# Optimization experiments

Measured on AMD Instinct MI355X. Metric: run time of the kernel, lower is better.

## Reference

```python
import math
import jax, jax.numpy as jnp
import numpy as np

N = 20000      # nodes
E = 320000     # edges
D_IN = 256
D_OUT = 256
H = 8
DK = D_OUT // H  # 32


def setup_inputs() -> dict:
    key = jax.random.key(0)
    ks = jax.random.split(key, 16)
    h = jax.random.normal(ks[0], (N, D_IN), dtype=jnp.float32)
    src = jax.random.randint(ks[1], (E,), 0, N, dtype=jnp.int32)
    dst = jax.random.randint(ks[2], (E,), 0, N, dtype=jnp.int32)
    s = 1.0 / math.sqrt(D_IN)
    Wk = jax.random.uniform(ks[3], (D_OUT, D_IN), jnp.float32, -s, s)
    bk = jnp.zeros((D_OUT,), jnp.float32)
    Wq = jax.random.uniform(ks[4], (D_OUT, D_IN), jnp.float32, -s, s)
    bq = jnp.zeros((D_OUT,), jnp.float32)
    Wv = jax.random.uniform(ks[5], (D_OUT, D_IN), jnp.float32, -s, s)
    bv = jnp.zeros((D_OUT,), jnp.float32)
    so = 1.0 / math.sqrt(D_OUT)
    Wa = jax.random.uniform(ks[6], (D_OUT, D_OUT), jnp.float32, -so, so)
    ba = jnp.zeros((D_OUT,), jnp.float32)
    # xavier_uniform over [n_rel=1, H, DK, DK]; fan_in = fan_out = DK
    bound = math.sqrt(6.0 / (DK + DK))
    rel_att = jax.random.uniform(ks[7], (H, DK, DK), jnp.float32, -bound, bound)
    rel_msg = jax.random.uniform(ks[8], (H, DK, DK), jnp.float32, -bound, bound)
    rel_pri = jnp.ones((H,), jnp.float32)
    skip = jnp.ones((), jnp.float32)
    return {"h": h, "src": src, "dst": dst, "Wk": Wk, "bk": bk, "Wq": Wq,
            "bq": bq, "Wv": Wv, "bv": bv, "Wa": Wa, "ba": ba,
            "rel_att": rel_att, "rel_msg": rel_msg, "rel_pri": rel_pri,
            "skip": skip}


def reference(h, src, dst, Wk, bk, Wq, bq, Wv, bv, Wa, ba, rel_att, rel_msg, rel_pri, skip):
    n = h.shape[0]
    sqrt_dk = math.sqrt(DK)
    # per-node projections, [N, H, DK]
    k = (h @ Wk.T + bk).reshape(n, H, DK)
    q = (h @ Wq.T + bq).reshape(n, H, DK)
    v = (h @ Wv.T + bv).reshape(n, H, DK)
    # relation-specific transforms (single relation, index 0)
    k = jnp.einsum('nhd,hde->nhe', k, rel_att)
    v = jnp.einsum('nhd,hde->nhe', v, rel_msg)
    # edge-wise dot-product score: v_dot_u(q_dst, k_src) -> [E, H]
    score = jnp.einsum('ehd,ehd->eh', q[dst], k[src]) * rel_pri / sqrt_dk
    # edge softmax normalized by dst
    m = jax.ops.segment_max(score, dst, num_segments=n)          # [N, H]
    ex = jnp.exp(score - m[dst])
    z = jax.ops.segment_sum(ex, dst, num_segments=n)             # [N, H]
    attn = ex / z[dst]                                           # [E, H]
    # weighted message aggregation: sum_e attn * v_src -> [N, H, DK]
    agg = jax.ops.segment_sum(v[src] * attn[:, :, None], dst, num_segments=n)
    t = agg.reshape(n, D_OUT)
    trans = t @ Wa.T + ba                                        # dropout = eval identity
    alpha = jax.nn.sigmoid(skip)
    return trans * alpha + h * (1.0 - alpha)
```

## Files before the change

kernel.cpp:

```cpp
#include <hip/hip_runtime.h>
#include <hip/hip_bf16.h>
#include <math.h>


#define NN   20000
#define NE   320000
#define MPAD 20096
#define DSTRIDE 96

typedef unsigned short u16;
typedef unsigned char  u8;
typedef __bf16 bf16x8 __attribute__((ext_vector_type(8)));
typedef u16    u16x8  __attribute__((ext_vector_type(8)));
typedef float  f32x4  __attribute__((ext_vector_type(4)));

__device__ __forceinline__ float bf2f(u16 x) {
    union { float f; unsigned u; } c; c.u = ((unsigned)x) << 16; return c.f;
}
__device__ __forceinline__ u16 f2bf(float f) {
    union { float f; unsigned u; } c; c.f = f;
    unsigned r = c.u + 0x7fffu + ((c.u >> 16) & 1u);
    return (u16)(r >> 16);
}

#if __has_builtin(__builtin_amdgcn_cvt_pk_fp8_f32) && __has_builtin(__builtin_amdgcn_cvt_pk_f32_fp8)
#define HWFP8 1
#else
#define HWFP8 0
#endif

__device__ __forceinline__ u8 f2fp8(float x) {
#if HWFP8
    return (u8)(__builtin_amdgcn_cvt_pk_fp8_f32(x, x, 0, false) & 0xff);
#else
    if (x != x) return 0x7f;
    unsigned sg = (x < 0.f) ? 0x80u : 0u;
    float a = fabsf(x); if (a > 448.f) a = 448.f;
    if (a < 0.015625f) {
        int m = (int)rintf(a * 512.f);
        if (m > 7) return (u8)(sg | 0x08);
        return (u8)(sg | m);
    }
    int e; (void)frexpf(a, &e);
    int p = e - 1;
    float mant = a * exp2f((float)(-p));
    int m = (int)rintf((mant - 1.f) * 8.f);
    int ef = p + 7;
    if (m == 8) { m = 0; ef++; }
    if (ef > 15) { ef = 15; m = 6; }
    return (u8)(sg | (ef << 3) | m);
#endif
}

__device__ __forceinline__ void fp8x4_dec(unsigned w, float* o) {
#if HWFP8
    auto lo = __builtin_amdgcn_cvt_pk_f32_fp8(w, false);
    auto hi = __builtin_amdgcn_cvt_pk_f32_fp8(w, true);
    o[0] = lo[0]; o[1] = lo[1]; o[2] = hi[0]; o[3] = hi[1];
#else
    #pragma unroll
    for (int j = 0; j < 4; ++j) {
        u8 b = (w >> (8 * j)) & 0xff;
        unsigned e = (b >> 3) & 15, m = b & 7;
        float v;
        if (e) { union { unsigned u; float f; } c; c.u = ((e + 120) << 23) | (m << 20); v = c.f; }
        else v = (float)m * 0.001953125f;
        o[j] = (b & 0x80) ? -v : v;
    }
#endif
}

__device__ __forceinline__ float fast_exp2(float x) {
#if __has_builtin(__builtin_amdgcn_exp2f)
    return __builtin_amdgcn_exp2f(x);
#else
    return exp2f(x);
#endif
}

__global__ void prep0(const float* __restrict__ Wq, const float* __restrict__ bq,
                      const float* __restrict__ Wk, const float* __restrict__ bk,
                      const float* __restrict__ Wv, const float* __restrict__ bv,
                      const float* __restrict__ Wa,
                      const float* __restrict__ rel_att, const float* __restrict__ rel_msg,
                      const float* __restrict__ rel_pri,
                      u16* __restrict__ W_all, float* __restrict__ b_eff,
                      u16* __restrict__ Wa_bf, int* __restrict__ cnt)
{
    const int bid = blockIdx.x, t = threadIdx.x;
    if (bid < 20) {
        const int i = bid * 256 + t;
        if (i < 5024) *(int4*)(cnt + i * 4) = make_int4(0, 0, 0, 0);
    } else if (bid < 788) {
        const int row = bid - 20, col = t;
        float val;
        if (row < 256) {
            val = Wq[row * 256 + col];
            if (col == 0) b_eff[row] = bq[row];
        } else {
            const int i = row - 256, g = i >> 7, o = i & 127;
            const bool isk = (o < 64);
            const int d = 64 * g + (isk ? o : o - 64);
            const int hh = d >> 5, e = d & 31;
            if (isk) {
                const float s = rel_pri[hh] * 0.17677669529663687f * 1.4426950408889634f;
                float acc = 0.f;
                for (int dd = 0; dd < 32; ++dd)
                    acc += rel_att[hh * 1024 + dd * 32 + e] * Wk[(hh * 32 + dd) * 256 + col];
                val = acc * s;
                if (col == 0) {
                    float b = 0.f;
                    for (int dd = 0; dd < 32; ++dd) b += rel_att[hh * 1024 + dd * 32 + e] * bk[hh * 32 + dd];
                    b_eff[row] = b * s;
                }
            } else {
                float acc = 0.f;
                for (int dd = 0; dd < 32; ++dd)
                    acc += rel_msg[hh * 1024 + dd * 32 + e] * Wv[(hh * 32 + dd) * 256 + col];
                val = acc;
                if (col == 0) {
                    float b = 0.f;
                    for (int dd = 0; dd < 32; ++dd) b += rel_msg[hh * 1024 + dd * 32 + e] * bv[hh * 32 + dd];
                    b_eff[row] = b;
                }
            }
        }
        W_all[row * 256 + col] = f2bf(val);
    } else {
        const int idx = (bid - 788) * 256 + t;
        Wa_bf[idx] = f2bf(Wa[idx]);
    }
}

__global__ __launch_bounds__(256) void gemm_qkv(
    const float* __restrict__ h, const u16* __restrict__ B,
    const float* __restrict__ bias, const int* __restrict__ src, const int* __restrict__ dst,
    u16* __restrict__ qb, u8* __restrict__ kv8, int* __restrict__ cnt, int* __restrict__ esrc)
{
    if (blockIdx.x >= 960) {
        const int e = (blockIdx.x - 960) * 256 + threadIdx.x;
        if (e < NE) {
            const int d = dst[e];
            const int p = atomicAdd(&cnt[d], 1);
            if (p < DSTRIDE) esrc[d * DSTRIDE + p] = src[e];
        }
        return;
    }
    const int xcd = blockIdx.x & 7, slot = blockIdx.x >> 3;
    const int rb = (slot % 20) * 8 + xcd;
    const int cb = slot / 20;
    if (rb >= 157) return;
    __shared__ u16 LDS[128 * 128];
    u16* At = LDS;
    u16* Bt = LDS + 128 * 64;
    const int t = threadIdx.x;
    const int wave = t >> 6, lane = t & 63;
    const int row0 = rb * 128, col0 = cb * 128;
    const int wm = (wave >> 1) * 64, wn = (wave & 1) * 64;
    const int cl = lane & 15, rh = lane >> 4;
    const int srow = t >> 3;
    const int lchunk = t & 7;
    const int swz = srow & 7;

    f32x4 acc[4][4] = {};
    float4 a0[4], a1[4];
    u16x8 bz[4];

    auto LOAD = [&](int k0) {
        #pragma unroll
        for (int r = 0; r < 4; ++r) {
            const int grow = row0 + r * 32 + srow;
            if (grow < NN) {
                a0[r] = *(const float4*)(h + (size_t)grow * 256 + k0 + lchunk * 8);
                a1[r] = *(const float4*)(h + (size_t)grow * 256 + k0 + lchunk * 8 + 4);
            } else {
                a0[r] = make_float4(0.f, 0.f, 0.f, 0.f);
                a1[r] = make_float4(0.f, 0.f, 0.f, 0.f);
            }
            bz[r] = *(const u16x8*)(B + (size_t)(col0 + r * 32 + srow) * 256 + k0 + lchunk * 8);
        }
    };
    auto COMMIT = [&]() {
        #pragma unroll
        for (int r = 0; r < 4; ++r) {
            u16x8 w8;
            w8[0] = f2bf(a0[r].x); w8[1] = f2bf(a0[r].y); w8[2] = f2bf(a0[r].z); w8[3] = f2bf(a0[r].w);
            w8[4] = f2bf(a1[r].x); w8[5] = f2bf(a1[r].y); w8[6] = f2bf(a1[r].z); w8[7] = f2bf(a1[r].w);
            *(u16x8*)&At[(r * 32 + srow) * 64 + (lchunk ^ swz) * 8] = w8;
            *(u16x8*)&Bt[(r * 32 + srow) * 64 + (lchunk ^ swz) * 8] = bz[r];
        }
    };

    LOAD(0);
    COMMIT();
    __syncthreads();
    #pragma unroll
    for (int ki = 0; ki < 4; ++ki) {
        if (ki < 3) LOAD((ki + 1) * 64);
        #pragma unroll
        for (int kk = 0; kk < 2; ++kk) {
            const int kc = kk * 4;
            bf16x8 af[4], bb[4];
            #pragma unroll
            for (int m = 0; m < 4; ++m) {
                const int ar = wm + 16 * m + cl;
                af[m] = *(const bf16x8*)&At[ar * 64 + (((kc + rh) ^ (ar & 7)) * 8)];
            }
            #pragma unroll
            for (int n = 0; n < 4; ++n) {
                const int br = wn + 16 * n + cl;
                bb[n] = *(const bf16x8*)&Bt[br * 64 + (((kc + rh) ^ (br & 7)) * 8)];
            }
            #pragma unroll
            for (int m = 0; m < 4; ++m)
                #pragma unroll
                for (int n = 0; n < 4; ++n)
                    acc[m][n] = __builtin_amdgcn_mfma_f32_16x16x32_bf16(af[m], bb[n], acc[m][n], 0, 0, 0);
        }
        __syncthreads();
        if (ki < 3) {
            COMMIT();
            __syncthreads();
        }
    }

    if (cb < 2) {
        #pragma unroll
        for (int n = 0; n < 4; ++n) {
            const int col = wn + 16 * n + cl;
            const float bv = bias[col0 + col];
            #pragma unroll
            for (int m = 0; m < 4; ++m) {
                const int rowb = wm + 16 * m + 4 * rh;
                #pragma unroll
                for (int r = 0; r < 4; ++r) {
                    const int row = rowb + r;
                    LDS[row * 128 + ((((col >> 3) ^ (row & 15)) << 3) | (col & 7))] =
                        f2bf(acc[m][n][r] + bv);
                }
            }
        }
        __syncthreads();
        #pragma unroll
        for (int it = 0; it < 8; ++it) {
            const int u = it * 256 + t;
            const int row = u >> 4, lc = u & 15;
            *(u16x8*)(qb + (size_t)(row0 + row) * 256 + col0 + lc * 8) =
                *(const u16x8*)&LDS[row * 128 + ((lc ^ (row & 15)) << 3)];
        }
    } else {
        u8* Cs8 = (u8*)LDS;
        const int g = cb - 2;
        #pragma unroll
        for (int n = 0; n < 4; ++n) {
            const int col = wn + 16 * n + cl;
            const float bv = bias[col0 + col];
            const int o = col & 63;
            const int p = ((o >> 3) << 4) + ((col < 64) ? 0 : 8) + (o & 7);
            #pragma unroll
            for (int m = 0; m < 4; ++m) {
                const int rowb = wm + 16 * m + 4 * rh;
                #pragma unroll
                for (int r = 0; r < 4; ++r) {
                    const int row = rowb + r;
                    Cs8[row * 128 + ((((p >> 3) ^ (row & 15)) << 3) | (p & 7))] =
                        f2fp8(acc[m][n][r] + bv);
                }
            }
        }
        __syncthreads();
        #pragma unroll
        for (int it = 0; it < 4; ++it) {
            const int u = it * 256 + t;
            const int row = u >> 3, un = u & 7;
            const uint2 a = *(const uint2*)&Cs8[row * 128 + (((2 * un) ^ (row & 15)) << 3)];
            const uint2 b = *(const uint2*)&Cs8[row * 128 + (((2 * un + 1) ^ (row & 15)) << 3)];
            *(uint4*)(kv8 + (size_t)(row0 + row) * 512 + g * 128 + un * 16) =
                make_uint4(a.x, a.y, b.x, b.y);
        }
    }
}

__global__ __launch_bounds__(256) void gemm_out(
    const u16* __restrict__ A, const u16* __restrict__ B,
    const float* __restrict__ bias, const float* __restrict__ hres,
    const float* __restrict__ skip, float* __restrict__ C)
{
    const int xcd = blockIdx.x & 7, slot = blockIdx.x >> 3;
    const int rb = (slot % 40) * 8 + xcd;
    const int cbo = slot / 40;
    if (rb >= 314) return;
    __shared__ u16 At[64 * 64];
    __shared__ u16 Bt[64 * 64];
    const int t = threadIdx.x;
    const int wave = t >> 6, lane = t & 63;
    const int row0 = rb * 64, col0 = cbo * 64;
    const int wm = (wave >> 1) * 32, wn = (wave & 1) * 32;
    const int cl = lane & 15, rh = lane >> 4;
    const int srow = t >> 3;
    const int lchunk = t & 7;
    const int swz = srow & 7;

    f32x4 acc[2][2] = {};
    u16x8 az[2], bz[2];

    auto LOAD = [&](int k0) {
        #pragma unroll
        for (int r = 0; r < 2; ++r) {
            az[r] = *(const u16x8*)(A + (size_t)(row0 + r * 32 + srow) * 256 + k0 + lchunk * 8);
            bz[r] = *(const u16x8*)(B + (size_t)(col0 + r * 32 + srow) * 256 + k0 + lchunk * 8);
        }
    };
    auto COMMIT = [&]() {
        #pragma unroll
        for (int r = 0; r < 2; ++r) {
            *(u16x8*)&At[(r * 32 + srow) * 64 + (lchunk ^ swz) * 8] = az[r];
            *(u16x8*)&Bt[(r * 32 + srow) * 64 + (lchunk ^ swz) * 8] = bz[r];
        }
    };

    LOAD(0);
    COMMIT();
    __syncthreads();
    #pragma unroll
    for (int ki = 0; ki < 4; ++ki) {
        if (ki < 3) LOAD((ki + 1) * 64);
        #pragma unroll
        for (int kk = 0; kk < 2; ++kk) {
            const int kc = kk * 4;
            bf16x8 af[2], bb[2];
            #pragma unroll
            for (int m = 0; m < 2; ++m) {
                const int ar = wm + 16 * m + cl;
                af[m] = *(const bf16x8*)&At[ar * 64 + (((kc + rh) ^ (ar & 7)) * 8)];
            }
            #pragma unroll
            for (int n = 0; n < 2; ++n) {
                const int br = wn + 16 * n + cl;
                bb[n] = *(const bf16x8*)&Bt[br * 64 + (((kc + rh) ^ (br & 7)) * 8)];
            }
            #pragma unroll
            for (int m = 0; m < 2; ++m)
                #pragma unroll
                for (int n = 0; n < 2; ++n)
                    acc[m][n] = __builtin_amdgcn_mfma_f32_16x16x32_bf16(af[m], bb[n], acc[m][n], 0, 0, 0);
        }
        __syncthreads();
        if (ki < 3) {
            COMMIT();
            __syncthreads();
        }
    }
    const float alpha = 1.f / (1.f + __expf(-skip[0]));
    const float beta = 1.f - alpha;
    #pragma unroll
    for (int n = 0; n < 2; ++n) {
        const int col = col0 + wn + 16 * n + cl;
        const float bv = bias[col];
        #pragma unroll
        for (int m = 0; m < 2; ++m) {
            const int rowb = row0 + wm + 16 * m + 4 * rh;
            #pragma unroll
            for (int r = 0; r < 4; ++r) {
                const int row = rowb + r;
                if (row < NN)
                    C[(size_t)row * 256 + col] =
                        (acc[m][n][r] + bv) * alpha + hres[(size_t)row * 256 + col] * beta;
            }
        }
    }
}

__device__ __forceinline__ void agg_w(uint4 w, const float* qf, float& z, float* acc)
{
    float kf[8], vf[8];
    fp8x4_dec(w.x, kf); fp8x4_dec(w.y, kf + 4);
    float s = 0.f;
    #pragma unroll
    for (int j = 0; j < 8; ++j) s += qf[j] * kf[j];
    s += __shfl_xor(s, 1);
    s += __shfl_xor(s, 2);
    const float ex = fast_exp2(s);
    z += ex;
    fp8x4_dec(w.z, vf); fp8x4_dec(w.w, vf + 4);
    #pragma unroll
    for (int j = 0; j < 8; ++j) acc[j] += ex * vf[j];
}

__global__ __launch_bounds__(256) void aggregate(
    const u16* __restrict__ qb, const u8* __restrict__ kv8, const int* __restrict__ cnt,
    const int* __restrict__ esrc, u16* __restrict__ tout)
{
    const int wid = blockIdx.x * 4 + (threadIdx.x >> 6);
    const int lane = threadIdx.x & 63;
    const int half = lane >> 5, sl = lane & 31;
    if (wid >= MPAD) return;
    if (wid >= NN) {
        if (half == 0) *(u16x8*)(tout + (size_t)wid * 256 + sl * 8) = (u16x8)0;
        return;
    }
    const u16x8 qv = *(const u16x8*)(qb + (size_t)wid * 256 + sl * 8);
    float qf[8];
    #pragma unroll
    for (int j = 0; j < 8; ++j) qf[j] = bf2f(qv[j]);
    float acc[8] = {0.f, 0.f, 0.f, 0.f, 0.f, 0.f, 0.f, 0.f};
    float z = 0.f;
    const int dcnt = min(cnt[wid], DSTRIDE);
    const int e0 = wid * DSTRIDE;
    for (int c0 = 0; c0 < dcnt; c0 += 64) {
        const int cn = min(64, dcnt - c0);
        const int jj = c0 + lane;
        const int myid = (jj < dcnt) ? esrc[e0 + jj] : 0;
        const int nfull = cn & ~15;
        int i = 0;
        for (; i < nfull; i += 16) {
            int idv[8];
            uint4 wreg[8];
            #pragma unroll
            for (int j = 0; j < 8; ++j) idv[j] = __shfl(myid, i + 2 * j + half);
            #pragma unroll
            for (int j = 0; j < 8; ++j)
                wreg[j] = *(const uint4*)(kv8 + (size_t)idv[j] * 512 + sl * 16);
            #pragma unroll
            for (int j = 0; j < 8; ++j) agg_w(wreg[j], qf, z, acc);
        }
        for (; i < cn; i += 2) {
            const int ii = i + half;
            const int id = __shfl(myid, ii);
            if (ii < cn) {
                const uint4 w = *(const uint4*)(kv8 + (size_t)id * 512 + sl * 16);
                agg_w(w, qf, z, acc);
            }
        }
    }
    #pragma unroll
    for (int j = 0; j < 8; ++j) acc[j] += __shfl_xor(acc[j], 32);
    z += __shfl_xor(z, 32);
    if (half == 0) {
        const float rz = (z > 0.f) ? 1.f / z : 0.f;
        u16x8 o;
        #pragma unroll
        for (int j = 0; j < 8; ++j) o[j] = f2bf(acc[j] * rz);
        *(u16x8*)(tout + (size_t)wid * 256 + sl * 8) = o;
    }
}

extern "C" void kernel_launch(void* const* d_in, const int* in_sizes, int n_in,
                              void* d_out, int out_size, void* d_ws, size_t ws_size,
                              hipStream_t stream)
{
    const float* h   = (const float*)d_in[0];
    const int*   src = (const int*)d_in[1];
    const int*   dst = (const int*)d_in[2];
    const float* Wk  = (const float*)d_in[3];
    const float* bk  = (const float*)d_in[4];
    const float* Wq  = (const float*)d_in[5];
    const float* bq  = (const float*)d_in[6];
    const float* Wv  = (const float*)d_in[7];
    const float* bv  = (const float*)d_in[8];
    const float* Wa  = (const float*)d_in[9];
    const float* ba  = (const float*)d_in[10];
    const float* rel_att = (const float*)d_in[11];
    const float* rel_msg = (const float*)d_in[12];
    const float* rel_pri = (const float*)d_in[13];
    const float* skip    = (const float*)d_in[14];
    float* out = (float*)d_out;

    char* w = (char*)d_ws;
    u16*   W_all = (u16*)(w + 0);
    float* b_eff = (float*)(w + 393216);
    u16*   Wa_bf = (u16*)(w + 396288);
    u16*   qb    = (u16*)(w + 527360);
    u8*    kv8   = (u8*)(w + 10816512);
    u16*   t_bf  = (u16*)(w + 21105664);
    int*   cnt   = (int*)(w + 31394816);
    int*   esrc  = (int*)(w + 31475200);

    prep0<<<1044, 256, 0, stream>>>(Wq, bq, Wk, bk, Wv, bv, Wa,
                                    rel_att, rel_msg, rel_pri,
                                    W_all, b_eff, Wa_bf, cnt);
    gemm_qkv<<<960 + 1250, 256, 0, stream>>>(h, W_all, b_eff, src, dst, qb, kv8, cnt, esrc);
    aggregate<<<MPAD / 4, 256, 0, stream>>>(qb, kv8, cnt, esrc, t_bf);
    gemm_out<<<1280, 256, 0, stream>>>(t_bf, Wa_bf, ba, h, skip, out);
}
```

Baseline: 91.35 us.

## Restructure QKV GEMM to 32-row tiles spanning all columns, split edge scatter

The QKV projection GEMM now gives each block 32 rows of h and loops over all 768 output columns. The A tile is loaded and converted to bf16 once, and the weight tiles are streamed through a double buffer. This removes the six-fold re-read and re-conversion of h across column blocks, and the q and kv8 outputs are written from one combined LDS staging step. The edge-bucketing scatter moves into its own kernel that handles four edges per thread with vector loads. The cost is smaller MFMA tiles per wave, more weight traffic per block, and an extra kernel launch.

After: 100.2 us. 9.7% more time.

```diff
diff --git a/kernel.cpp b/kernel.cpp
--- a/kernel.cpp
+++ b/kernel.cpp
@@ -132,152 +132,146 @@
     }
 }
 
-__global__ __launch_bounds__(256) void gemm_qkv(
+__global__ void scatter_edges(const int* __restrict__ dst, const int* __restrict__ src,
+                              int* __restrict__ cnt, int* __restrict__ esrc)
+{
+    const int e0 = (blockIdx.x * 256 + threadIdx.x) * 4;
+    if (e0 >= NE) return;
+    const int4 d4 = *(const int4*)(dst + e0);
+    const int4 s4 = *(const int4*)(src + e0);
+    const int p0 = atomicAdd(&cnt[d4.x], 1);
+    const int p1 = atomicAdd(&cnt[d4.y], 1);
+    const int p2 = atomicAdd(&cnt[d4.z], 1);
+    const int p3 = atomicAdd(&cnt[d4.w], 1);
+    if (p0 < DSTRIDE) esrc[d4.x * DSTRIDE + p0] = s4.x;
+    if (p1 < DSTRIDE) esrc[d4.y * DSTRIDE + p1] = s4.y;
+    if (p2 < DSTRIDE) esrc[d4.z * DSTRIDE + p2] = s4.z;
+    if (p3 < DSTRIDE) esrc[d4.w * DSTRIDE + p3] = s4.w;
+}
+
+__global__ __launch_bounds__(256, 3) void gemm_qkv(
     const float* __restrict__ h, const u16* __restrict__ B,
-    const float* __restrict__ bias, const int* __restrict__ src, const int* __restrict__ dst,
-    u16* __restrict__ qb, u8* __restrict__ kv8, int* __restrict__ cnt, int* __restrict__ esrc)
-{
-    if (blockIdx.x >= 960) {
-        const int e = (blockIdx.x - 960) * 256 + threadIdx.x;
-        if (e < NE) {
-            const int d = dst[e];
-            const int p = atomicAdd(&cnt[d], 1);
-            if (p < DSTRIDE) esrc[d * DSTRIDE + p] = src[e];
-        }
-        return;
-    }
-    const int xcd = blockIdx.x & 7, slot = blockIdx.x >> 3;
-    const int rb = (slot % 20) * 8 + xcd;
-    const int cb = slot / 20;
-    if (rb >= 157) return;
-    __shared__ u16 LDS[128 * 128];
-    u16* At = LDS;
-    u16* Bt = LDS + 128 * 64;
+    const float* __restrict__ bias, u16* __restrict__ qb, u8* __restrict__ kv8)
+{
+    __shared__ u16 LDS[24576];
     const int t = threadIdx.x;
     const int wave = t >> 6, lane = t & 63;
-    const int row0 = rb * 128, col0 = cb * 128;
-    const int wm = (wave >> 1) * 64, wn = (wave & 1) * 64;
     const int cl = lane & 15, rh = lane >> 4;
-    const int srow = t >> 3;
-    const int lchunk = t & 7;
-    const int swz = srow & 7;
-
-    f32x4 acc[4][4] = {};
-    float4 a0[4], a1[4];
-    u16x8 bz[4];
-
-    auto LOAD = [&](int k0) {
-        #pragma unroll
-        for (int r = 0; r < 4; ++r) {
-            const int grow = row0 + r * 32 + srow;
+    const int row0 = blockIdx.x * 32;
+    const int ar_ = t >> 3;
+    const int lc = t & 7;
+
+    f32x4 acc[6][2][2] = {};
+    u16x8 breg[4];
+
+    {
+        const int grow = row0 + ar_;
+        #pragma unroll
+        for (int kb = 0; kb < 4; ++kb) {
+            u16x8 w8 = (u16x8)0;
             if (grow < NN) {
-                a0[r] = *(const float4*)(h + (size_t)grow * 256 + k0 + lchunk * 8);
-                a1[r] = *(const float4*)(h + (size_t)grow * 256 + k0 + lchunk * 8 + 4);
-            } else {
-                a0[r] = make_float4(0.f, 0.f, 0.f, 0.f);
-                a1[r] = make_float4(0.f, 0.f, 0.f, 0.f);
-            }
-            bz[r] = *(const u16x8*)(B + (size_t)(col0 + r * 32 + srow) * 256 + k0 + lchunk * 8);
+                const float4 f0 = *(const float4*)(h + (size_t)grow * 256 + kb * 64 + lc * 8);
+                const float4 f1 = *(const float4*)(h + (size_t)grow * 256 + kb * 64 + lc * 8 + 4);
+                w8[0] = f2bf(f0.x); w8[1] = f2bf(f0.y); w8[2] = f2bf(f0.z); w8[3] = f2bf(f0.w);
+                w8[4] = f2bf(f1.x); w8[5] = f2bf(f1.y); w8[6] = f2bf(f1.z); w8[7] = f2bf(f1.w);
+            }
+            *(u16x8*)&LDS[kb * 2048 + ar_ * 64 + ((lc ^ (ar_ & 7)) * 8)] = w8;
+        }
+    }
+
+    auto LOADB = [&](int cb, int kc) {
+        #pragma unroll
+        for (int i = 0; i < 4; ++i) {
+            const int u = i * 256 + t;
+            const int brow = u >> 3, ch = u & 7;
+            breg[i] = *(const u16x8*)(B + (size_t)(cb * 128 + brow) * 256 + kc * 64 + ch * 8);
         }
     };
-    auto COMMIT = [&]() {
-        #pragma unroll
-        for (int r = 0; r < 4; ++r) {
-            u16x8 w8;
-            w8[0] = f2bf(a0[r].x); w8[1] = f2bf(a0[r].y); w8[2] = f2bf(a0[r].z); w8[3] = f2bf(a0[r].w);
-            w8[4] = f2bf(a1[r].x); w8[5] = f2bf(a1[r].y); w8[6] = f2bf(a1[r].z); w8[7] = f2bf(a1[r].w);
-            *(u16x8*)&At[(r * 32 + srow) * 64 + (lchunk ^ swz) * 8] = w8;
-            *(u16x8*)&Bt[(r * 32 + srow) * 64 + (lchunk ^ swz) * 8] = bz[r];
+    auto COMMITB = [&](int buf) {
+        u16* Bt = &LDS[8192 + buf * 8192];
+        #pragma unroll
+        for (int i = 0; i < 4; ++i) {
+            const int u = i * 256 + t;
+            const int brow = u >> 3, ch = u & 7;
+            *(u16x8*)&Bt[brow * 64 + ((ch ^ (brow & 7)) * 8)] = breg[i];
         }
     };
 
-    LOAD(0);
-    COMMIT();
+    LOADB(0, 0);
+    COMMITB(0);
     __syncthreads();
-    #pragma unroll
-    for (int ki = 0; ki < 4; ++ki) {
-        if (ki < 3) LOAD((ki + 1) * 64);
+
+    #pragma unroll
+    for (int s = 0; s < 24; ++s) {
+        const int cb = s >> 2, kc = s & 3;
+        if (s < 23) LOADB((s + 1) >> 2, (s + 1) & 3);
+        const u16* Bt = &LDS[8192 + (s & 1) * 8192];
         #pragma unroll
         for (int kk = 0; kk < 2; ++kk) {
-            const int kc = kk * 4;
-            bf16x8 af[4], bb[4];
-            #pragma unroll
-            for (int m = 0; m < 4; ++m) {
-                const int ar = wm + 16 * m + cl;
-                af[m] = *(const bf16x8*)&At[ar * 64 + (((kc + rh) ^ (ar & 7)) * 8)];
-            }
-            #pragma unroll
-            for (int n = 0; n < 4; ++n) {
-                const int br = wn + 16 * n + cl;
-                bb[n] = *(const bf16x8*)&Bt[br * 64 + (((kc + rh) ^ (br & 7)) * 8)];
-            }
-            #pragma unroll
-            for (int m = 0; m < 4; ++m)
+            bf16x8 af[2], bb[2];
+            #pragma unroll
+            for (int m = 0; m < 2; ++m) {
+                const int ar = 16 * m + cl;
+                af[m] = *(const bf16x8*)&LDS[kc * 2048 + ar * 64 + (((kk * 4 + rh) ^ (ar & 7)) * 8)];
+            }
+            #pragma unroll
+            for (int n = 0; n < 2; ++n) {
+                const int br = wave * 32 + 16 * n + cl;
+                bb[n] = *(const bf16x8*)&Bt[br * 64 + (((kk * 4 + rh) ^ (br & 7)) * 8)];
+            }
+            #pragma unroll
+            for (int m = 0; m < 2; ++m)
                 #pragma unroll
-                for (int n = 0; n < 4; ++n)
-                    acc[m][n] = __builtin_amdgcn_mfma_f32_16x16x32_bf16(af[m], bb[n], acc[m][n], 0, 0, 0);
-        }
+                for (int n = 0; n < 2; ++n)
+                    acc[cb][m][n] = __builtin_amdgcn_mfma_f32_16x16x32_bf16(af[m], bb[n], acc[cb][m][n], 0, 0, 0);
+        }
+        if (s < 23) COMMITB((s + 1) & 1);
         __syncthreads();
-        if (ki < 3) {
-            COMMIT();
-            __syncthreads();
-        }
-    }
-
-    if (cb < 2) {
-        #pragma unroll
-        for (int n = 0; n < 4; ++n) {
-            const int col = wn + 16 * n + cl;
-            const float bv = bias[col0 + col];
-            #pragma unroll
-            for (int m = 0; m < 4; ++m) {
-                const int rowb = wm + 16 * m + 4 * rh;
+    }
+
+    u16* Cq = LDS;
+    u8*  Ckv = (u8*)&LDS[8192];
+    #pragma unroll
+    for (int cb = 0; cb < 6; ++cb) {
+        #pragma unroll
+        for (int n = 0; n < 2; ++n) {
+            const int colg = cb * 128 + wave * 32 + 16 * n + cl;
+            const float bv = bias[colg];
+            #pragma unroll
+            for (int m = 0; m < 2; ++m) {
                 #pragma unroll
-                for (int r = 0; r < 4; ++r) {
-                    const int row = rowb + r;
-                    LDS[row * 128 + ((((col >> 3) ^ (row & 15)) << 3) | (col & 7))] =
-                        f2bf(acc[m][n][r] + bv);
+                for (int r2 = 0; r2 < 4; ++r2) {
+                    const int row = 16 * m + 4 * rh + r2;
+                    const float val = acc[cb][m][n][r2] + bv;
+                    if (cb < 2) {
+                        const int ch = colg >> 3;
+                        const int phys = (ch & 24) | ((ch ^ row) & 7);
+                        Cq[row * 256 + phys * 8 + (colg & 7)] = f2bf(val);
+                    } else {
+                        const int g = cb - 2, c = colg & 127, o = c & 63;
+                        const int p = g * 128 + ((o >> 3) << 4) + ((c < 64) ? 0 : 8) + (o & 7);
+                        const int ch = p >> 4;
+                        const int phys = (ch & 24) | ((ch ^ row) & 7);
+                        Ckv[row * 512 + phys * 16 + (p & 15)] = f2fp8(val);
+                    }
                 }
             }
         }
-        __syncthreads();
-        #pragma unroll
-        for (int it = 0; it < 8; ++it) {
-            const int u = it * 256 + t;
-            const int row = u >> 4, lc = u & 15;
-            *(u16x8*)(qb + (size_t)(row0 + row) * 256 + col0 + lc * 8) =
-                *(const u16x8*)&LDS[row * 128 + ((lc ^ (row & 15)) << 3)];
-        }
-    } else {
-        u8* Cs8 = (u8*)LDS;
-        const int g = cb - 2;
-        #pragma unroll
-        for (int n = 0; n < 4; ++n) {
-            const int col = wn + 16 * n + cl;
-            const float bv = bias[col0 + col];
-            const int o = col & 63;
-            const int p = ((o >> 3) << 4) + ((col < 64) ? 0 : 8) + (o & 7);
-            #pragma unroll
-            for (int m = 0; m < 4; ++m) {
-                const int rowb = wm + 16 * m + 4 * rh;
-                #pragma unroll
-                for (int r = 0; r < 4; ++r) {
-                    const int row = rowb + r;
-                    Cs8[row * 128 + ((((p >> 3) ^ (row & 15)) << 3) | (p & 7))] =
-                        f2fp8(acc[m][n][r] + bv);
-                }
-            }
-        }
-        __syncthreads();
-        #pragma unroll
-        for (int it = 0; it < 4; ++it) {
-            const int u = it * 256 + t;
-            const int row = u >> 3, un = u & 7;
-            const uint2 a = *(const uint2*)&Cs8[row * 128 + (((2 * un) ^ (row & 15)) << 3)];
-            const uint2 b = *(const uint2*)&Cs8[row * 128 + (((2 * un + 1) ^ (row & 15)) << 3)];
-            *(uint4*)(kv8 + (size_t)(row0 + row) * 512 + g * 128 + un * 16) =
-                make_uint4(a.x, a.y, b.x, b.y);
-        }
+    }
+    __syncthreads();
+    #pragma unroll
+    for (int i = 0; i < 4; ++i) {
+        const int u = i * 256 + t;
+        const int row = u >> 5, ch = u & 31;
+        const int phys = (ch & 24) | ((ch ^ row) & 7);
+        *(u16x8*)(qb + (size_t)(row0 + row) * 256 + ch * 8) = *(const u16x8*)&Cq[row * 256 + phys * 8];
+    }
+    #pragma unroll
+    for (int i = 0; i < 4; ++i) {
+        const int u = i * 256 + t;
+        const int row = u >> 5, ch = u & 31;
+        const int phys = (ch & 24) | ((ch ^ row) & 7);
+        *(uint4*)(kv8 + (size_t)(row0 + row) * 512 + ch * 16) = *(const uint4*)&Ckv[row * 512 + phys * 16];
     }
 }
 
@@ -479,7 +473,8 @@
     prep0<<<1044, 256, 0, stream>>>(Wq, bq, Wk, bk, Wv, bv, Wa,
                                     rel_att, rel_msg, rel_pri,
                                     W_all, b_eff, Wa_bf, cnt);
-    gemm_qkv<<<960 + 1250, 256, 0, stream>>>(h, W_all, b_eff, src, dst, qb, kv8, cnt, esrc);
+    scatter_edges<<<313, 256, 0, stream>>>(dst, src, cnt, esrc);
+    gemm_qkv<<<628, 256, 0, stream>>>(h, W_all, b_eff, qb, kv8);
     aggregate<<<MPAD / 4, 256, 0, stream>>>(qb, kv8, cnt, esrc, t_bf);
     gemm_out<<<1280, 256, 0, stream>>>(t_bf, Wa_bf, ba, h, skip, out);
 }
```
